# Performance work log

Hardware: AMD Instinct MI355X
Metric: run time of the kernel (lower is better)

Reference implementation:

```python
import jax, jax.numpy as jnp
import numpy as np
from numpy.polynomial import Polynomial

B, C = 2000000, 10
EXP = dict(start=0.0, stop=1.0, n=1000, deg=8)
INV = dict(start=10.0, stop=30.0, n=1000, deg=4)
LOG = dict(start=0.01, stop=0.5, n=1000, deg=8)
ITERATIONS = 3


def _fit(fn, start, stop, n, deg):
    x = np.linspace(start, stop, n)
    return Polynomial.fit(x, fn(x), deg).convert(kind=Polynomial).coef.astype(np.float32)


def _polyval(coeffs, x):
    # Horner; coeffs ascending order (numpy Polynomial convention)
    res = jnp.full_like(x, coeffs[-1])
    for i in range(coeffs.shape[0] - 2, -1, -1):
        res = res * x + coeffs[i]
    return res


def setup_inputs() -> dict:
    key = jax.random.key(0)
    k1, k2 = jax.random.split(key)
    enc_input = jax.random.uniform(k1, (B, C), dtype=jnp.float32)  # logits in [0,1)
    labels = jax.random.randint(k2, (B,), 0, C)
    enc_target = jax.nn.one_hot(labels, C, dtype=jnp.float32)
    exp_coeffs = jnp.asarray(_fit(np.exp, **{'start': EXP['start'], 'stop': EXP['stop'], 'n': EXP['n'], 'deg': EXP['deg']}))
    inverse_coeffs = jnp.asarray(_fit(lambda x: 1.0 / x, INV['start'], INV['stop'], INV['n'], INV['deg']))
    log_coeffs = jnp.asarray(_fit(np.log, LOG['start'], LOG['stop'], LOG['n'], LOG['deg']))
    return {
        'enc_input': enc_input,
        'enc_target': enc_target,
        'exp_coeffs': exp_coeffs,
        'inverse_coeffs': inverse_coeffs,
        'log_coeffs': log_coeffs,
        'iterations': ITERATIONS,
    }


def reference(enc_input, enc_target, exp_coeffs, inverse_coeffs, log_coeffs, iterations):
    # exp via polynomial approximation (Horner / ciphertext poly eval)
    e = _polyval(exp_coeffs, enc_input)                      # [B, C]
    s = jnp.sum(e, axis=1, keepdims=True)                    # [B, 1]
    # inverse via polynomial initial guess + Newton-Raphson refinement
    inv = _polyval(inverse_coeffs, s)
    for _ in range(iterations):
        inv = inv * (2.0 - s * inv)
    softmax = e * inv                                        # [B, C]
    log_softmax = _polyval(log_coeffs, softmax)              # [B, C]
    # mean cross-entropy over the batch
    loss = -jnp.sum(enc_target * log_softmax) / enc_input.shape[0]
    return loss


if __name__ == '__main__':
    out = reference(**setup_inputs())
    print(out)
```

## Files before the change

kernel.cpp:

```cpp
#include <hip/hip_runtime.h>

#define CCOL 10
#define TPB 256
#define NBLOCKS 1024

typedef float v4f __attribute__((ext_vector_type(4)));
#define NT(p) __builtin_nontemporal_load(p)

__device__ __forceinline__ float horner9(const float c[9], float x) {
    float v = c[8];
#pragma unroll
    for (int i = 7; i >= 0; i--) v = fmaf(v, x, c[i]);
    return v;
}

#define EXP4(v, base)                          \
    e[(base) + 0] = horner9(ec, (v).x);        \
    e[(base) + 1] = horner9(ec, (v).y);        \
    e[(base) + 2] = horner9(ec, (v).z);        \
    e[(base) + 3] = horner9(ec, (v).w);

#define LOG4(tv, base)                                                    \
    {                                                                     \
        float i0 = ((base) + 0 < CCOL) ? inv0 : inv1;                     \
        float i1 = ((base) + 1 < CCOL) ? inv0 : inv1;                     \
        float i2 = ((base) + 2 < CCOL) ? inv0 : inv1;                     \
        float i3 = ((base) + 3 < CCOL) ? inv0 : inv1;                     \
        local = fmaf((tv).x, horner9(lc, e[(base) + 0] * i0), local);     \
        local = fmaf((tv).y, horner9(lc, e[(base) + 1] * i1), local);     \
        local = fmaf((tv).z, horner9(lc, e[(base) + 2] * i2), local);     \
        local = fmaf((tv).w, horner9(lc, e[(base) + 3] * i3), local);     \
    }

__global__ __launch_bounds__(TPB, 4) void ce_kernel(
    const float* __restrict__ x, const float* __restrict__ tgt,
    const float* __restrict__ exp_c, const float* __restrict__ inv_c,
    const float* __restrict__ log_c, const int* __restrict__ iters_p,
    float* __restrict__ partials, int npairs, int nchunks)
{
    __shared__ v4f lds4[2560];

    float ec[9], ic[5], lc[9];
#pragma unroll
    for (int i = 0; i < 9; i++) ec[i] = exp_c[i];
#pragma unroll
    for (int i = 0; i < 5; i++) ic[i] = inv_c[i];
#pragma unroll
    for (int i = 0; i < 9; i++) lc[i] = log_c[i];
    const int niter = iters_p[0];

    const int tid  = threadIdx.x;
    const int lane = tid & 63;
    const int w    = tid >> 6;
    const int wg   = blockIdx.x * 4 + w;
    const int W    = gridDim.x * 4;

    v4f* lx = lds4 + w * 640;
    v4f* lt = lx + 320;
    const v4f* bx = (const v4f*)((const float*)lx + lane * 20);
    const v4f* bt = (const v4f*)((const float*)lt + lane * 20);

    float local = 0.0f;

    int q = wg;
    v4f rx0, rx1, rx2, rx3, rx4, rt0, rt1, rt2, rt3, rt4;
    if (q < nchunks) {
        const v4f* gx = (const v4f*)x   + (size_t)q * 320 + lane;
        const v4f* gt = (const v4f*)tgt + (size_t)q * 320 + lane;
        rx0 = NT(gx); rx1 = NT(gx + 64); rx2 = NT(gx + 128); rx3 = NT(gx + 192); rx4 = NT(gx + 256);
        rt0 = NT(gt); rt1 = NT(gt + 64); rt2 = NT(gt + 128); rt3 = NT(gt + 192); rt4 = NT(gt + 256);
    }

    while (q < nchunks) {
        v4f* sx = lx + lane;
        sx[0] = rx0; sx[64] = rx1; sx[128] = rx2; sx[192] = rx3; sx[256] = rx4;
        v4f* st = lt + lane;
        st[0] = rt0; st[64] = rt1; st[128] = rt2; st[192] = rt3; st[256] = rt4;

        int qn = q + W;
        if (qn < nchunks) {
            const v4f* gx = (const v4f*)x   + (size_t)qn * 320 + lane;
            const v4f* gt = (const v4f*)tgt + (size_t)qn * 320 + lane;
            rx0 = NT(gx); rx1 = NT(gx + 64); rx2 = NT(gx + 128); rx3 = NT(gx + 192); rx4 = NT(gx + 256);
            rt0 = NT(gt); rt1 = NT(gt + 64); rt2 = NT(gt + 128); rt3 = NT(gt + 192); rt4 = NT(gt + 256);
        }

        v4f a0 = bx[0], a1 = bx[1], a2 = bx[2], a3 = bx[3], a4 = bx[4];
        float e[2 * CCOL];
        EXP4(a0, 0) EXP4(a1, 4) EXP4(a2, 8) EXP4(a3, 12) EXP4(a4, 16)

        float s0 = 0.0f, s1 = 0.0f;
#pragma unroll
        for (int i = 0; i < CCOL; i++) s0 += e[i];
#pragma unroll
        for (int i = CCOL; i < 2 * CCOL; i++) s1 += e[i];

        float inv0 = ic[4], inv1 = ic[4];
#pragma unroll
        for (int k = 3; k >= 0; k--) {
            inv0 = fmaf(inv0, s0, ic[k]);
            inv1 = fmaf(inv1, s1, ic[k]);
        }
        for (int k = 0; k < niter; k++) {
            inv0 = inv0 * (2.0f - s0 * inv0);
            inv1 = inv1 * (2.0f - s1 * inv1);
        }

        v4f t0 = bt[0], t1 = bt[1], t2 = bt[2], t3 = bt[3], t4 = bt[4];
        LOG4(t0, 0) LOG4(t1, 4) LOG4(t2, 8) LOG4(t3, 12) LOG4(t4, 16)

        q = qn;
    }

    int tail0 = nchunks * 64;
    for (int p = tail0 + blockIdx.x * TPB + tid; p < npairs; p += gridDim.x * TPB) {
        const float* xp = x   + (size_t)p * 2 * CCOL;
        const float* tp = tgt + (size_t)p * 2 * CCOL;
#pragma unroll
        for (int r = 0; r < 2; r++) {
            float e2[CCOL], s = 0.0f;
#pragma unroll
            for (int c = 0; c < CCOL; c++) {
                float v = horner9(ec, xp[r * CCOL + c]);
                e2[c] = v; s += v;
            }
            float inv = ic[4];
#pragma unroll
            for (int k = 3; k >= 0; k--) inv = fmaf(inv, s, ic[k]);
            for (int k = 0; k < niter; k++) inv = inv * (2.0f - s * inv);
#pragma unroll
            for (int c = 0; c < CCOL; c++)
                local = fmaf(tp[r * CCOL + c], horner9(lc, e2[c] * inv), local);
        }
    }

#pragma unroll
    for (int off = 32; off > 0; off >>= 1)
        local += __shfl_down(local, off, 64);

    __syncthreads();
    float* wsum = (float*)lds4;
    if (lane == 0) wsum[w] = local;
    __syncthreads();
    if (tid == 0)
        partials[blockIdx.x] = wsum[0] + wsum[1] + wsum[2] + wsum[3];
}

__global__ __launch_bounds__(TPB) void reduce_kernel(
    const float* __restrict__ partials, float* __restrict__ out, float neg_inv_b)
{
    int tid = threadIdx.x;
    float local = 0.0f;
#pragma unroll
    for (int k = 0; k < NBLOCKS / TPB; k++)
        local += partials[tid + k * TPB];
#pragma unroll
    for (int off = 32; off > 0; off >>= 1)
        local += __shfl_down(local, off, 64);
    __shared__ float wsum[4];
    if ((tid & 63) == 0) wsum[tid >> 6] = local;
    __syncthreads();
    if (tid == 0)
        out[0] = (wsum[0] + wsum[1] + wsum[2] + wsum[3]) * neg_inv_b;
}

extern "C" void kernel_launch(void* const* d_in, const int* in_sizes, int n_in,
                              void* d_out, int out_size, void* d_ws, size_t ws_size,
                              hipStream_t stream) {
    const float* x  = (const float*)d_in[0];
    const float* t  = (const float*)d_in[1];
    const float* ec = (const float*)d_in[2];
    const float* ic = (const float*)d_in[3];
    const float* lc = (const float*)d_in[4];
    const int*   it = (const int*)d_in[5];
    float* out = (float*)d_out;
    float* partials = (float*)d_ws;

    int b_rows = in_sizes[0] / CCOL;
    int npairs = b_rows / 2;
    int nchunks = npairs / 64;
    float neg_inv_b = -1.0f / (float)b_rows;

    ce_kernel<<<NBLOCKS, TPB, 0, stream>>>(x, t, ec, ic, lc, it, partials,
                                           npairs, nchunks);
    reduce_kernel<<<1, TPB, 0, stream>>>(partials, out, neg_inv_b);
}
```

Baseline: 168.0 us.

## Deepen register prefetch to two chunks ahead and lower block occupancy

Each wave now prefetches two chunks ahead with two ping-ponged register buffer sets, so two chunks of global loads are in flight while it computes the current one. The launch bound drops from 4 to 3 blocks per SIMD and the grid shrinks from 1024 to 768 blocks to leave room for the extra registers. The aim is to hide memory latency on this bandwidth-bound stream. The cost is fewer resident waves, and register pressure could cause spills.

```diff
diff --git a/kernel.cpp b/kernel.cpp
--- a/kernel.cpp
+++ b/kernel.cpp
@@ -2,7 +2,7 @@
 
 #define CCOL 10
 #define TPB 256
-#define NBLOCKS 1024
+#define NBLOCKS 768
 
 typedef float v4f __attribute__((ext_vector_type(4)));
 #define NT(p) __builtin_nontemporal_load(p)
@@ -32,7 +32,49 @@
         local = fmaf((tv).w, horner9(lc, e[(base) + 3] * i3), local);     \
     }
 
-__global__ __launch_bounds__(TPB, 4) void ce_kernel(
+#define LOAD_CHUNK(qq, X0, X1, X2, X3, X4, T0, T1, T2, T3, T4)            \
+    {                                                                     \
+        const v4f* gx = (const v4f*)x   + (size_t)(qq) * 320 + lane;      \
+        const v4f* gt = (const v4f*)tgt + (size_t)(qq) * 320 + lane;      \
+        X0 = NT(gx);       X1 = NT(gx + 64);  X2 = NT(gx + 128);          \
+        X3 = NT(gx + 192); X4 = NT(gx + 256);                             \
+        T0 = NT(gt);       T1 = NT(gt + 64);  T2 = NT(gt + 128);          \
+        T3 = NT(gt + 192); T4 = NT(gt + 256);                             \
+    }
+
+#define STAGE_CHUNK(X0, X1, X2, X3, X4, T0, T1, T2, T3, T4)               \
+    {                                                                     \
+        v4f* sx = lx + lane;                                              \
+        sx[0] = X0; sx[64] = X1; sx[128] = X2; sx[192] = X3; sx[256] = X4;\
+        v4f* st = lt + lane;                                              \
+        st[0] = T0; st[64] = T1; st[128] = T2; st[192] = T3; st[256] = T4;\
+    }
+
+#define COMPUTE_CHUNK()                                                   \
+    {                                                                     \
+        v4f a0 = bx[0], a1 = bx[1], a2 = bx[2], a3 = bx[3], a4 = bx[4];   \
+        float e[2 * CCOL];                                                \
+        EXP4(a0, 0) EXP4(a1, 4) EXP4(a2, 8) EXP4(a3, 12) EXP4(a4, 16)    \
+        float s0 = 0.0f, s1 = 0.0f;                                       \
+        _Pragma("unroll")                                                 \
+        for (int i = 0; i < CCOL; i++) s0 += e[i];                        \
+        _Pragma("unroll")                                                 \
+        for (int i = CCOL; i < 2 * CCOL; i++) s1 += e[i];                 \
+        float inv0 = ic[4], inv1 = ic[4];                                 \
+        _Pragma("unroll")                                                 \
+        for (int k = 3; k >= 0; k--) {                                    \
+            inv0 = fmaf(inv0, s0, ic[k]);                                 \
+            inv1 = fmaf(inv1, s1, ic[k]);                                 \
+        }                                                                 \
+        for (int k = 0; k < niter; k++) {                                 \
+            inv0 = inv0 * (2.0f - s0 * inv0);                             \
+            inv1 = inv1 * (2.0f - s1 * inv1);                             \
+        }                                                                 \
+        v4f t0 = bt[0], t1 = bt[1], t2 = bt[2], t3 = bt[3], t4 = bt[4];   \
+        LOG4(t0, 0) LOG4(t1, 4) LOG4(t2, 8) LOG4(t3, 12) LOG4(t4, 16)    \
+    }
+
+__global__ __launch_bounds__(TPB, 3) void ce_kernel(
     const float* __restrict__ x, const float* __restrict__ tgt,
     const float* __restrict__ exp_c, const float* __restrict__ inv_c,
     const float* __restrict__ log_c, const int* __restrict__ iters_p,
@@ -62,54 +104,26 @@
 
     float local = 0.0f;
 
+    v4f ax0, ax1, ax2, ax3, ax4, at0, at1, at2, at3, at4;
+    v4f px0, px1, px2, px3, px4, pt0, pt1, pt2, pt3, pt4;
+
     int q = wg;
-    v4f rx0, rx1, rx2, rx3, rx4, rt0, rt1, rt2, rt3, rt4;
-    if (q < nchunks) {
-        const v4f* gx = (const v4f*)x   + (size_t)q * 320 + lane;
-        const v4f* gt = (const v4f*)tgt + (size_t)q * 320 + lane;
-        rx0 = NT(gx); rx1 = NT(gx + 64); rx2 = NT(gx + 128); rx3 = NT(gx + 192); rx4 = NT(gx + 256);
-        rt0 = NT(gt); rt1 = NT(gt + 64); rt2 = NT(gt + 128); rt3 = NT(gt + 192); rt4 = NT(gt + 256);
-    }
+    if (q < nchunks)     LOAD_CHUNK(q,     ax0, ax1, ax2, ax3, ax4, at0, at1, at2, at3, at4);
+    if (q + W < nchunks) LOAD_CHUNK(q + W, px0, px1, px2, px3, px4, pt0, pt1, pt2, pt3, pt4);
 
     while (q < nchunks) {
-        v4f* sx = lx + lane;
-        sx[0] = rx0; sx[64] = rx1; sx[128] = rx2; sx[192] = rx3; sx[256] = rx4;
-        v4f* st = lt + lane;
-        st[0] = rt0; st[64] = rt1; st[128] = rt2; st[192] = rt3; st[256] = rt4;
-
-        int qn = q + W;
-        if (qn < nchunks) {
-            const v4f* gx = (const v4f*)x   + (size_t)qn * 320 + lane;
-            const v4f* gt = (const v4f*)tgt + (size_t)qn * 320 + lane;
-            rx0 = NT(gx); rx1 = NT(gx + 64); rx2 = NT(gx + 128); rx3 = NT(gx + 192); rx4 = NT(gx + 256);
-            rt0 = NT(gt); rt1 = NT(gt + 64); rt2 = NT(gt + 128); rt3 = NT(gt + 192); rt4 = NT(gt + 256);
-        }
-
-        v4f a0 = bx[0], a1 = bx[1], a2 = bx[2], a3 = bx[3], a4 = bx[4];
-        float e[2 * CCOL];
-        EXP4(a0, 0) EXP4(a1, 4) EXP4(a2, 8) EXP4(a3, 12) EXP4(a4, 16)
-
-        float s0 = 0.0f, s1 = 0.0f;
-#pragma unroll
-        for (int i = 0; i < CCOL; i++) s0 += e[i];
-#pragma unroll
-        for (int i = CCOL; i < 2 * CCOL; i++) s1 += e[i];
-
-        float inv0 = ic[4], inv1 = ic[4];
-#pragma unroll
-        for (int k = 3; k >= 0; k--) {
-            inv0 = fmaf(inv0, s0, ic[k]);
-            inv1 = fmaf(inv1, s1, ic[k]);
-        }
-        for (int k = 0; k < niter; k++) {
-            inv0 = inv0 * (2.0f - s0 * inv0);
-            inv1 = inv1 * (2.0f - s1 * inv1);
-        }
-
-        v4f t0 = bt[0], t1 = bt[1], t2 = bt[2], t3 = bt[3], t4 = bt[4];
-        LOG4(t0, 0) LOG4(t1, 4) LOG4(t2, 8) LOG4(t3, 12) LOG4(t4, 16)
-
-        q = qn;
+        STAGE_CHUNK(ax0, ax1, ax2, ax3, ax4, at0, at1, at2, at3, at4);
+        if (q + 2 * W < nchunks)
+            LOAD_CHUNK(q + 2 * W, ax0, ax1, ax2, ax3, ax4, at0, at1, at2, at3, at4);
+        COMPUTE_CHUNK();
+        q += W;
+        if (q >= nchunks) break;
+
+        STAGE_CHUNK(px0, px1, px2, px3, px4, pt0, pt1, pt2, pt3, pt4);
+        if (q + 2 * W < nchunks)
+            LOAD_CHUNK(q + 2 * W, px0, px1, px2, px3, px4, pt0, pt1, pt2, pt3, pt4);
+        COMPUTE_CHUNK();
+        q += W;
     }
 
     int tail0 = nchunks * 64;
```

New measurement: 169.0 us. Within noise of the previous version (+0.6%).
